# Kernel optimization log

Measured on AMD Instinct MI355X. Metric: run time of the kernel, lower is better.

Reference implementation:

```python
import jax, jax.numpy as jnp
import numpy as np

LOG2 = float(np.log(2.0))
CUTOFF = 10.0
INPUT_DIM = 5


def ssp(x):
    # ShiftedSoftplus
    return jax.nn.softplus(x) - LOG2


def setup_inputs() -> dict:
    key = jax.random.key(0)
    ks = jax.random.split(key, 16)
    N, E, D, G, L = 20000, 320000, 128, 100, 6
    s = 0.05
    return {
        "z": jax.random.normal(ks[0], (N, INPUT_DIM + D), jnp.float32),
        "edge_index": jax.random.randint(ks[1], (2, E), 0, N, dtype=jnp.int64),
        "edge_length": jax.random.uniform(ks[2], (E,), jnp.float32),
        "edge_attr": jax.random.uniform(ks[3], (E, G), jnp.float32),
        "emblin_w": jax.random.normal(ks[4], (D, INPUT_DIM), jnp.float32) * s,
        "emblin_b": jnp.zeros((D,), jnp.float32),
        "mlp_w1": jax.random.normal(ks[5], (L, D, G), jnp.float32) * s,
        "mlp_b1": jnp.zeros((L, D), jnp.float32),
        "mlp_w2": jax.random.normal(ks[6], (L, D, D), jnp.float32) * s,
        "mlp_b2": jnp.zeros((L, D), jnp.float32),
        "lin1_w": jax.random.normal(ks[7], (L, D, D), jnp.float32) * s,
        "lin2_w": jax.random.normal(ks[8], (L, D, D), jnp.float32) * s,
        "lin2_b": jnp.zeros((L, D), jnp.float32),
        "lin_w": jax.random.normal(ks[9], (L, D, 2 * D), jnp.float32) * s,
        "lin_b": jnp.zeros((L, D), jnp.float32),
    }


def reference(z, edge_index, edge_length, edge_attr, emblin_w, emblin_b,
              mlp_w1, mlp_b1, mlp_w2, mlp_b2, lin1_w, lin2_w, lin2_b,
              lin_w, lin_b):
    # time_emb=True path: split z into node features and time embedding
    zf, ptemb = z[:, :INPUT_DIM], z[:, INPUT_DIM:]
    h = zf @ emblin_w.T + emblin_b + ptemb          # [N, D]
    src, dst = edge_index[0], edge_index[1]
    N = h.shape[0]
    # non-smooth cutoff gate: C = (edge_length <= cutoff)
    C = (edge_length <= CUTOFF).astype(h.dtype)     # [E]
    L = mlp_w1.shape[0]
    for l in range(L):
        # edge-wise filter MLP with cutoff gate
        Wf = ssp(edge_attr @ mlp_w1[l].T + mlp_b1[l]) @ mlp_w2[l].T + mlp_b2[l]
        Wf = Wf * C[:, None]                        # [E, F]
        xf = h @ lin1_w[l].T                        # [N, F]
        m_ij = xf[src] * Wf                         # gather + elementwise, [E, F]
        m_i = jax.ops.segment_sum(m_ij, dst, num_segments=N)  # scatter-add, [N, F]
        m = ssp(m_i @ lin2_w[l].T + lin2_b[l])      # [N, D]
        h = h + (jnp.concatenate([h, m], axis=1) @ lin_w[l].T + lin_b[l])
    return h
```

## Files before the change

kernel.cpp:

```cpp
#include <hip/hip_runtime.h>

#define N_NODES 20000
#define D 128
#define E_EDGES 320000
#define G 100
#define L_LAYERS 6
#define IN_DIM 5
#define ZROW (IN_DIM + D)
#define CUTOFF_V 10.0f
#define LOG2F_ 0.69314718055994530942f

typedef __attribute__((ext_vector_type(8))) short bf16x8;
typedef __attribute__((ext_vector_type(4))) float f32x4;
typedef unsigned short ushort_t;
typedef unsigned int uint_t;

__device__ __forceinline__ float sspf(float x) {
    return fmaxf(x, 0.0f) + __logf(1.0f + __expf(-fabsf(x))) - LOG2F_;
}

__device__ __forceinline__ ushort_t f2bf(float f) {
    union { float f; uint_t u; } x; x.f = f;
    uint_t r = ((x.u >> 16) & 1u) + 0x7fffu;
    return (ushort_t)((x.u + r) >> 16);
}

__device__ __forceinline__ uint_t pack2(float a, float b) {
    return (uint_t)f2bf(a) | ((uint_t)f2bf(b) << 16);
}

__device__ __forceinline__ f32x4 mfma_bf16(bf16x8 a, bf16x8 b, f32x4 c) {
    return __builtin_amdgcn_mfma_f32_16x16x32_bf16(a, b, c, 0, 0, 0);
}

__global__ void embed_kernel(const float* __restrict__ z,
                             const float* __restrict__ ew,
                             const float* __restrict__ eb,
                             float* __restrict__ h) {
    int n = blockIdx.x;
    int d = threadIdx.x;
    const float* zr = z + (size_t)n * ZROW;
    float acc = eb[d] + zr[IN_DIM + d];
#pragma unroll
    for (int k = 0; k < IN_DIM; ++k) acc += zr[k] * ew[d * IN_DIM + k];
    h[(size_t)n * D + d] = acc;
}

__global__ void convw1_kernel(const float* __restrict__ w1, ushort_t* __restrict__ out) {
    int idx = blockIdx.x * 256 + threadIdx.x;
    int k = idx & 127;
    int nl = idx >> 7;
    out[idx] = (k < G) ? f2bf(w1[(size_t)nl * G + k]) : (ushort_t)0;
}

__global__ void castbf_kernel(const float* __restrict__ src, ushort_t* __restrict__ dst) {
    int i = blockIdx.x * 256 + threadIdx.x;
    dst[i] = f2bf(src[i]);
}

__global__ void hist_kernel(const int* __restrict__ ei, int* __restrict__ deg) {
    int e = blockIdx.x * 256 + threadIdx.x;
    atomicAdd(&deg[ei[E_EDGES + e]], 1);
}

__global__ __launch_bounds__(1024) void scan_kernel(const int* __restrict__ deg,
                                                    int* __restrict__ row_start,
                                                    int* __restrict__ cursor) {
    __shared__ int wsum[16];
    int t = threadIdx.x;
    const int CH = (N_NODES + 1023) / 1024;
    int base = t * CH;
    int s = 0;
    for (int i = 0; i < CH; ++i) {
        int idx = base + i;
        if (idx < N_NODES) s += deg[idx];
    }
    int lane = t & 63, wid = t >> 6;
    int v = s;
    for (int o = 1; o < 64; o <<= 1) {
        int u = __shfl_up(v, o, 64);
        if (lane >= o) v += u;
    }
    if (lane == 63) wsum[wid] = v;
    __syncthreads();
    if (t == 0) {
        int acc = 0;
        for (int i = 0; i < 16; ++i) { int tmp = wsum[i]; wsum[i] = acc; acc += tmp; }
    }
    __syncthreads();
    int run = v - s + wsum[wid];
    for (int i = 0; i < CH; ++i) {
        int idx = base + i;
        if (idx < N_NODES) {
            row_start[idx] = run;
            cursor[idx] = run;
            run += deg[idx];
        }
    }
    if (t == 0) row_start[N_NODES] = E_EDGES;
}

__global__ void scatter_perm_kernel(const int* __restrict__ ei, const float* __restrict__ el,
                                    int* __restrict__ cursor,
                                    int* __restrict__ perm, int* __restrict__ src_p,
                                    float* __restrict__ cm_p) {
    int e = blockIdx.x * 256 + threadIdx.x;
    int d = ei[E_EDGES + e];
    int p = atomicAdd(&cursor[d], 1);
    perm[p] = e;
    src_p[p] = ei[e];
    cm_p[p] = (el[e] <= CUTOFF_V) ? 1.0f : 0.0f;
}

__global__ void attr_perm_kernel(const float* __restrict__ edge_attr,
                                 const int* __restrict__ perm,
                                 ushort_t* __restrict__ attr_p) {
    int tid = blockIdx.x * 256 + threadIdx.x;
    int r = tid >> 5, ch = tid & 31;
    float4 v = make_float4(0.f, 0.f, 0.f, 0.f);
    if (ch < 25) {
        int pe = perm[r];
        v = *(const float4*)(edge_attr + (size_t)pe * G + ch * 4);
    }
    uint2 p; p.x = pack2(v.x, v.y); p.y = pack2(v.z, v.w);
    *(uint2*)(attr_p + (size_t)r * 128 + ch * 4) = p;
}

__global__ __launch_bounds__(256) void edge_mlp_kernel(
    const ushort_t* __restrict__ attr_p, const float* __restrict__ cm_p,
    const ushort_t* __restrict__ w1b, const float* __restrict__ b1,
    const ushort_t* __restrict__ w2b, const float* __restrict__ b2,
    ushort_t* __restrict__ wf) {
    __shared__ __align__(16) ushort_t sT[32][136];

    int t = threadIdx.x, lane = t & 63, wid = t >> 6;
    int c = lane & 15, quad = lane >> 4;
    int er0 = blockIdx.x * 32;
    int mbase = wid * 32;

    f32x4 acc[2][2];
#pragma unroll
    for (int st = 0; st < 2; ++st)
#pragma unroll
        for (int ct = 0; ct < 2; ++ct) acc[st][ct] = (f32x4){0.f, 0.f, 0.f, 0.f};

#pragma unroll
    for (int ks = 0; ks < 4; ++ks) {
        int koff = ks * 32 + quad * 8;
        bf16x8 b0  = *(const bf16x8*)(attr_p + (size_t)(er0 + c) * 128 + koff);
        bf16x8 b1v = *(const bf16x8*)(attr_p + (size_t)(er0 + 16 + c) * 128 + koff);
#pragma unroll
        for (int ct = 0; ct < 2; ++ct) {
            bf16x8 a = *(const bf16x8*)(w1b + (size_t)(mbase + ct * 16 + c) * 128 + koff);
            acc[0][ct] = mfma_bf16(a, b0, acc[0][ct]);
            acc[1][ct] = mfma_bf16(a, b1v, acc[1][ct]);
        }
    }
#pragma unroll
    for (int st = 0; st < 2; ++st)
#pragma unroll
        for (int ct = 0; ct < 2; ++ct) {
            int col = mbase + ct * 16 + quad * 4;
            float4 bv = *(const float4*)(b1 + col);
            uint2 p;
            p.x = pack2(sspf(acc[st][ct][0] + bv.x), sspf(acc[st][ct][1] + bv.y));
            p.y = pack2(sspf(acc[st][ct][2] + bv.z), sspf(acc[st][ct][3] + bv.w));
            *(uint2*)(&sT[st * 16 + c][col]) = p;
        }

    __syncthreads();

#pragma unroll
    for (int st = 0; st < 2; ++st)
#pragma unroll
        for (int ct = 0; ct < 2; ++ct) acc[st][ct] = (f32x4){0.f, 0.f, 0.f, 0.f};
#pragma unroll
    for (int ks = 0; ks < 4; ++ks) {
        int koff = ks * 32 + quad * 8;
        bf16x8 b0  = *(const bf16x8*)(&sT[c][koff]);
        bf16x8 b1v = *(const bf16x8*)(&sT[16 + c][koff]);
#pragma unroll
        for (int ct = 0; ct < 2; ++ct) {
            bf16x8 a = *(const bf16x8*)(w2b + (size_t)(mbase + ct * 16 + c) * 128 + koff);
            acc[0][ct] = mfma_bf16(a, b0, acc[0][ct]);
            acc[1][ct] = mfma_bf16(a, b1v, acc[1][ct]);
        }
    }
#pragma unroll
    for (int st = 0; st < 2; ++st) {
        int e = er0 + st * 16 + c;
        float cv = cm_p[e];
#pragma unroll
        for (int ct = 0; ct < 2; ++ct) {
            int col = mbase + ct * 16 + quad * 4;
            float4 bv = *(const float4*)(b2 + col);
            uint2 p;
            p.x = pack2((acc[st][ct][0] + bv.x) * cv, (acc[st][ct][1] + bv.y) * cv);
            p.y = pack2((acc[st][ct][2] + bv.z) * cv, (acc[st][ct][3] + bv.w) * cv);
            *(uint2*)(wf + (size_t)e * 128 + col) = p;
        }
    }
}

template <bool HASB, bool SSP, bool RES, bool BF16OUT, bool TWOK>
__global__ __launch_bounds__(256) void node_mfma_kernel(
    const float* __restrict__ in0, const float* __restrict__ in1,
    const ushort_t* __restrict__ Wb, const float* __restrict__ bias,
    const float* __restrict__ resid, void* __restrict__ outp) {
    __shared__ __align__(16) ushort_t sT[32][136];
    const int WS = TWOK ? 256 : 128;
    int t = threadIdx.x, lane = t & 63, wid = t >> 6;
    int c = lane & 15, quad = lane >> 4;
    int n0 = blockIdx.x * 32;
    int mbase = wid * 32;

    f32x4 acc[2][2];
#pragma unroll
    for (int st = 0; st < 2; ++st)
#pragma unroll
        for (int ct = 0; ct < 2; ++ct) acc[st][ct] = (f32x4){0.f, 0.f, 0.f, 0.f};

    const float* src = in0;
#pragma unroll 1
    for (int ph = 0; ph < (TWOK ? 2 : 1); ++ph) {
        if (ph) __syncthreads();
#pragma unroll
        for (int i = 0; i < 4; ++i) {
            int idx = i * 256 + t;
            int r = idx >> 5, ch = idx & 31;
            int gr = n0 + r;
            float4 v = make_float4(0.f, 0.f, 0.f, 0.f);
            if (gr < N_NODES) v = *(const float4*)(src + (size_t)gr * 128 + ch * 4);
            uint2 p; p.x = pack2(v.x, v.y); p.y = pack2(v.z, v.w);
            *(uint2*)(&sT[r][ch * 4]) = p;
        }
        __syncthreads();
        int kb = ph * 128;
#pragma unroll
        for (int ks = 0; ks < 4; ++ks) {
            int koff = ks * 32 + quad * 8;
            bf16x8 b0  = *(const bf16x8*)(&sT[c][koff]);
            bf16x8 b1v = *(const bf16x8*)(&sT[16 + c][koff]);
#pragma unroll
            for (int ct = 0; ct < 2; ++ct) {
                bf16x8 a = *(const bf16x8*)(Wb + (size_t)(mbase + ct * 16 + c) * WS + kb + koff);
                acc[0][ct] = mfma_bf16(a, b0, acc[0][ct]);
                acc[1][ct] = mfma_bf16(a, b1v, acc[1][ct]);
            }
        }
        src = in1;
    }

#pragma unroll
    for (int st = 0; st < 2; ++st) {
        int node = n0 + st * 16 + c;
        if (node < N_NODES) {
#pragma unroll
            for (int ct = 0; ct < 2; ++ct) {
                int col = mbase + ct * 16 + quad * 4;
                float4 bv = make_float4(0.f, 0.f, 0.f, 0.f);
                if (HASB) bv = *(const float4*)(bias + col);
                float v0 = acc[st][ct][0] + bv.x;
                float v1 = acc[st][ct][1] + bv.y;
                float v2 = acc[st][ct][2] + bv.z;
                float v3 = acc[st][ct][3] + bv.w;
                if (SSP) { v0 = sspf(v0); v1 = sspf(v1); v2 = sspf(v2); v3 = sspf(v3); }
                if (RES) {
                    float4 rv = *(const float4*)(resid + (size_t)node * 128 + col);
                    v0 += rv.x; v1 += rv.y; v2 += rv.z; v3 += rv.w;
                }
                if (BF16OUT) {
                    uint2 p; p.x = pack2(v0, v1); p.y = pack2(v2, v3);
                    *(uint2*)((ushort_t*)outp + (size_t)node * 128 + col) = p;
                } else {
                    *(float4*)((float*)outp + (size_t)node * 128 + col) =
                        make_float4(v0, v1, v2, v3);
                }
            }
        }
    }
}

__global__ __launch_bounds__(256) void segsum_kernel(
    const ushort_t* __restrict__ wf, const ushort_t* __restrict__ xf_bf,
    const int* __restrict__ row_start, const int* __restrict__ src_p,
    float* __restrict__ m_i) {
    int t = threadIdx.x, lane = t & 63;
    int n = blockIdx.x * 4 + (t >> 6);
    int beg = row_start[n], end = row_start[n + 1];
    float a0 = 0.f, a1 = 0.f;
    for (int i = beg; i < end; ++i) {
        uint_t w = *(const uint_t*)(wf + (size_t)i * 128 + lane * 2);
        uint_t x = *(const uint_t*)(xf_bf + (size_t)src_p[i] * 128 + lane * 2);
        a0 += __uint_as_float(w << 16) * __uint_as_float(x << 16);
        a1 += __uint_as_float(w & 0xffff0000u) * __uint_as_float(x & 0xffff0000u);
    }
    *(float2*)(m_i + (size_t)n * 128 + lane * 2) = make_float2(a0, a1);
}

extern "C" void kernel_launch(void* const* d_in, const int* in_sizes, int n_in,
                              void* d_out, int out_size, void* d_ws, size_t ws_size,
                              hipStream_t stream) {
    const float* z        = (const float*)d_in[0];
    const int*   ei       = (const int*)d_in[1];
    const float* el       = (const float*)d_in[2];
    const float* ea       = (const float*)d_in[3];
    const float* emblin_w = (const float*)d_in[4];
    const float* emblin_b = (const float*)d_in[5];
    const float* mlp_w1   = (const float*)d_in[6];
    const float* mlp_b1   = (const float*)d_in[7];
    const float* mlp_w2   = (const float*)d_in[8];
    const float* mlp_b2   = (const float*)d_in[9];
    const float* lin1_w   = (const float*)d_in[10];
    const float* lin2_w   = (const float*)d_in[11];
    const float* lin2_b   = (const float*)d_in[12];
    const float* lin_w    = (const float*)d_in[13];
    const float* lin_b    = (const float*)d_in[14];
    (void)in_sizes; (void)n_in; (void)out_size; (void)ws_size;

    const size_t ND = (size_t)N_NODES * D;
    float* ws   = (float*)d_ws;
    float* h    = ws;
    float* m_i  = h + ND;
    float* cm_p = m_i + ND;
    float* fend = cm_p + E_EDGES;

    ushort_t* w1b    = (ushort_t*)fend;
    ushort_t* w2b    = w1b   + (size_t)L_LAYERS * D * 128;
    ushort_t* lin1b  = w2b   + (size_t)L_LAYERS * D * D;
    ushort_t* lin2b  = lin1b + (size_t)L_LAYERS * D * D;
    ushort_t* linwb  = lin2b + (size_t)L_LAYERS * D * D;
    ushort_t* wf     = linwb + (size_t)L_LAYERS * D * 256;
    ushort_t* xf_bf  = wf    + (size_t)E_EDGES * 128;
    ushort_t* attr_p = xf_bf + ND;
    int* ibase      = (int*)(attr_p + (size_t)E_EDGES * 128);
    int* deg        = ibase;
    int* row_start  = deg + N_NODES;
    int* cursor     = row_start + N_NODES + 1;
    int* perm       = cursor + N_NODES;
    int* src_p      = perm + E_EDGES;

    convw1_kernel<<<(L_LAYERS * D * 128) / 256, 256, 0, stream>>>(mlp_w1, w1b);
    castbf_kernel<<<(L_LAYERS * D * D) / 256, 256, 0, stream>>>(mlp_w2, w2b);
    castbf_kernel<<<(L_LAYERS * D * D) / 256, 256, 0, stream>>>(lin1_w, lin1b);
    castbf_kernel<<<(L_LAYERS * D * D) / 256, 256, 0, stream>>>(lin2_w, lin2b);
    castbf_kernel<<<(L_LAYERS * D * 256) / 256, 256, 0, stream>>>(lin_w, linwb);

    hipMemsetAsync(deg, 0, (size_t)N_NODES * sizeof(int), stream);
    hist_kernel<<<E_EDGES / 256, 256, 0, stream>>>(ei, deg);
    scan_kernel<<<1, 1024, 0, stream>>>(deg, row_start, cursor);
    scatter_perm_kernel<<<E_EDGES / 256, 256, 0, stream>>>(ei, el, cursor, perm, src_p, cm_p);
    attr_perm_kernel<<<(E_EDGES * 32) / 256, 256, 0, stream>>>(ea, perm, attr_p);

    embed_kernel<<<N_NODES, D, 0, stream>>>(z, emblin_w, emblin_b, h);

    const int NBLK = (N_NODES + 31) / 32;
    for (int l = 0; l < L_LAYERS; ++l) {
        node_mfma_kernel<false, false, false, true, false><<<NBLK, 256, 0, stream>>>(
            h, nullptr, lin1b + (size_t)l * D * D, nullptr, nullptr, xf_bf);
        edge_mlp_kernel<<<E_EDGES / 32, 256, 0, stream>>>(
            attr_p, cm_p, w1b + (size_t)l * D * 128, mlp_b1 + (size_t)l * D,
            w2b + (size_t)l * D * D, mlp_b2 + (size_t)l * D, wf);
        segsum_kernel<<<N_NODES / 4, 256, 0, stream>>>(wf, xf_bf, row_start, src_p, m_i);
        node_mfma_kernel<true, true, false, false, false><<<NBLK, 256, 0, stream>>>(
            m_i, nullptr, lin2b + (size_t)l * D * D, lin2_b + (size_t)l * D,
            nullptr, m_i);
        node_mfma_kernel<true, false, true, false, true><<<NBLK, 256, 0, stream>>>(
            h, m_i, linwb + (size_t)l * D * 256, lin_b + (size_t)l * D, h, h);
    }

    hipMemcpyAsync(d_out, h, ND * sizeof(float), hipMemcpyDeviceToDevice, stream);
}
```

Baseline: 1.522 ms.

## Fuse lin2 and update GEMMs into one tail kernel; widen edge MLP waves

Merges the lin2+ssp node GEMM and the concat update GEMM into one kernel that keeps the ssp output in shared memory as bf16. This removes a kernel launch and the fp32 round trip of m_i through global memory. Separately, the edge MLP kernel now runs 2 waves of 128 threads, each covering 64 output columns instead of 32, so each block uses fewer threads and each thread holds more accumulators. In-place write of h is safe because each block reads only its own rows before writing them.

Result: faster. 1.401 ms (-8.0%).

```diff
diff --git a/kernel.cpp b/kernel.cpp
--- a/kernel.cpp
+++ b/kernel.cpp
@@ -126,7 +126,7 @@
     *(uint2*)(attr_p + (size_t)r * 128 + ch * 4) = p;
 }
 
-__global__ __launch_bounds__(256) void edge_mlp_kernel(
+__global__ __launch_bounds__(128) void edge_mlp_kernel(
     const ushort_t* __restrict__ attr_p, const float* __restrict__ cm_p,
     const ushort_t* __restrict__ w1b, const float* __restrict__ b1,
     const ushort_t* __restrict__ w2b, const float* __restrict__ b2,
@@ -136,13 +136,13 @@
     int t = threadIdx.x, lane = t & 63, wid = t >> 6;
     int c = lane & 15, quad = lane >> 4;
     int er0 = blockIdx.x * 32;
-    int mbase = wid * 32;
-
-    f32x4 acc[2][2];
-#pragma unroll
-    for (int st = 0; st < 2; ++st)
-#pragma unroll
-        for (int ct = 0; ct < 2; ++ct) acc[st][ct] = (f32x4){0.f, 0.f, 0.f, 0.f};
+    int mbase = wid * 64;
+
+    f32x4 acc[2][4];
+#pragma unroll
+    for (int st = 0; st < 2; ++st)
+#pragma unroll
+        for (int ct = 0; ct < 4; ++ct) acc[st][ct] = (f32x4){0.f, 0.f, 0.f, 0.f};
 
 #pragma unroll
     for (int ks = 0; ks < 4; ++ks) {
@@ -150,7 +150,7 @@
         bf16x8 b0  = *(const bf16x8*)(attr_p + (size_t)(er0 + c) * 128 + koff);
         bf16x8 b1v = *(const bf16x8*)(attr_p + (size_t)(er0 + 16 + c) * 128 + koff);
 #pragma unroll
-        for (int ct = 0; ct < 2; ++ct) {
+        for (int ct = 0; ct < 4; ++ct) {
             bf16x8 a = *(const bf16x8*)(w1b + (size_t)(mbase + ct * 16 + c) * 128 + koff);
             acc[0][ct] = mfma_bf16(a, b0, acc[0][ct]);
             acc[1][ct] = mfma_bf16(a, b1v, acc[1][ct]);
@@ -159,7 +159,7 @@
 #pragma unroll
     for (int st = 0; st < 2; ++st)
 #pragma unroll
-        for (int ct = 0; ct < 2; ++ct) {
+        for (int ct = 0; ct < 4; ++ct) {
             int col = mbase + ct * 16 + quad * 4;
             float4 bv = *(const float4*)(b1 + col);
             uint2 p;
@@ -173,14 +173,14 @@
 #pragma unroll
     for (int st = 0; st < 2; ++st)
 #pragma unroll
-        for (int ct = 0; ct < 2; ++ct) acc[st][ct] = (f32x4){0.f, 0.f, 0.f, 0.f};
+        for (int ct = 0; ct < 4; ++ct) acc[st][ct] = (f32x4){0.f, 0.f, 0.f, 0.f};
 #pragma unroll
     for (int ks = 0; ks < 4; ++ks) {
         int koff = ks * 32 + quad * 8;
         bf16x8 b0  = *(const bf16x8*)(&sT[c][koff]);
         bf16x8 b1v = *(const bf16x8*)(&sT[16 + c][koff]);
 #pragma unroll
-        for (int ct = 0; ct < 2; ++ct) {
+        for (int ct = 0; ct < 4; ++ct) {
             bf16x8 a = *(const bf16x8*)(w2b + (size_t)(mbase + ct * 16 + c) * 128 + koff);
             acc[0][ct] = mfma_bf16(a, b0, acc[0][ct]);
             acc[1][ct] = mfma_bf16(a, b1v, acc[1][ct]);
@@ -191,7 +191,7 @@
         int e = er0 + st * 16 + c;
         float cv = cm_p[e];
 #pragma unroll
-        for (int ct = 0; ct < 2; ++ct) {
+        for (int ct = 0; ct < 4; ++ct) {
             int col = mbase + ct * 16 + quad * 4;
             float4 bv = *(const float4*)(b2 + col);
             uint2 p;
@@ -202,13 +202,10 @@
     }
 }
 
-template <bool HASB, bool SSP, bool RES, bool BF16OUT, bool TWOK>
-__global__ __launch_bounds__(256) void node_mfma_kernel(
-    const float* __restrict__ in0, const float* __restrict__ in1,
-    const ushort_t* __restrict__ Wb, const float* __restrict__ bias,
-    const float* __restrict__ resid, void* __restrict__ outp) {
+__global__ __launch_bounds__(256) void lin1_kernel(
+    const float* __restrict__ in0, const ushort_t* __restrict__ Wb,
+    ushort_t* __restrict__ outp) {
     __shared__ __align__(16) ushort_t sT[32][136];
-    const int WS = TWOK ? 256 : 128;
     int t = threadIdx.x, lane = t & 63, wid = t >> 6;
     int c = lane & 15, quad = lane >> 4;
     int n0 = blockIdx.x * 32;
@@ -220,35 +217,28 @@
 #pragma unroll
         for (int ct = 0; ct < 2; ++ct) acc[st][ct] = (f32x4){0.f, 0.f, 0.f, 0.f};
 
-    const float* src = in0;
-#pragma unroll 1
-    for (int ph = 0; ph < (TWOK ? 2 : 1); ++ph) {
-        if (ph) __syncthreads();
-#pragma unroll
-        for (int i = 0; i < 4; ++i) {
-            int idx = i * 256 + t;
-            int r = idx >> 5, ch = idx & 31;
-            int gr = n0 + r;
-            float4 v = make_float4(0.f, 0.f, 0.f, 0.f);
-            if (gr < N_NODES) v = *(const float4*)(src + (size_t)gr * 128 + ch * 4);
-            uint2 p; p.x = pack2(v.x, v.y); p.y = pack2(v.z, v.w);
-            *(uint2*)(&sT[r][ch * 4]) = p;
-        }
-        __syncthreads();
-        int kb = ph * 128;
-#pragma unroll
-        for (int ks = 0; ks < 4; ++ks) {
-            int koff = ks * 32 + quad * 8;
-            bf16x8 b0  = *(const bf16x8*)(&sT[c][koff]);
-            bf16x8 b1v = *(const bf16x8*)(&sT[16 + c][koff]);
-#pragma unroll
-            for (int ct = 0; ct < 2; ++ct) {
-                bf16x8 a = *(const bf16x8*)(Wb + (size_t)(mbase + ct * 16 + c) * WS + kb + koff);
-                acc[0][ct] = mfma_bf16(a, b0, acc[0][ct]);
-                acc[1][ct] = mfma_bf16(a, b1v, acc[1][ct]);
-            }
-        }
-        src = in1;
+#pragma unroll
+    for (int i = 0; i < 4; ++i) {
+        int idx = i * 256 + t;
+        int r = idx >> 5, ch = idx & 31;
+        int gr = n0 + r;
+        float4 v = make_float4(0.f, 0.f, 0.f, 0.f);
+        if (gr < N_NODES) v = *(const float4*)(in0 + (size_t)gr * 128 + ch * 4);
+        uint2 p; p.x = pack2(v.x, v.y); p.y = pack2(v.z, v.w);
+        *(uint2*)(&sT[r][ch * 4]) = p;
+    }
+    __syncthreads();
+#pragma unroll
+    for (int ks = 0; ks < 4; ++ks) {
+        int koff = ks * 32 + quad * 8;
+        bf16x8 b0  = *(const bf16x8*)(&sT[c][koff]);
+        bf16x8 b1v = *(const bf16x8*)(&sT[16 + c][koff]);
+#pragma unroll
+        for (int ct = 0; ct < 2; ++ct) {
+            bf16x8 a = *(const bf16x8*)(Wb + (size_t)(mbase + ct * 16 + c) * 128 + koff);
+            acc[0][ct] = mfma_bf16(a, b0, acc[0][ct]);
+            acc[1][ct] = mfma_bf16(a, b1v, acc[1][ct]);
+        }
     }
 
 #pragma unroll
@@ -258,24 +248,123 @@
 #pragma unroll
             for (int ct = 0; ct < 2; ++ct) {
                 int col = mbase + ct * 16 + quad * 4;
-                float4 bv = make_float4(0.f, 0.f, 0.f, 0.f);
-                if (HASB) bv = *(const float4*)(bias + col);
-                float v0 = acc[st][ct][0] + bv.x;
-                float v1 = acc[st][ct][1] + bv.y;
-                float v2 = acc[st][ct][2] + bv.z;
-                float v3 = acc[st][ct][3] + bv.w;
-                if (SSP) { v0 = sspf(v0); v1 = sspf(v1); v2 = sspf(v2); v3 = sspf(v3); }
-                if (RES) {
-                    float4 rv = *(const float4*)(resid + (size_t)node * 128 + col);
-                    v0 += rv.x; v1 += rv.y; v2 += rv.z; v3 += rv.w;
-                }
-                if (BF16OUT) {
-                    uint2 p; p.x = pack2(v0, v1); p.y = pack2(v2, v3);
-                    *(uint2*)((ushort_t*)outp + (size_t)node * 128 + col) = p;
-                } else {
-                    *(float4*)((float*)outp + (size_t)node * 128 + col) =
-                        make_float4(v0, v1, v2, v3);
-                }
+                uint2 p;
+                p.x = pack2(acc[st][ct][0], acc[st][ct][1]);
+                p.y = pack2(acc[st][ct][2], acc[st][ct][3]);
+                *(uint2*)(outp + (size_t)node * 128 + col) = p;
+            }
+        }
+    }
+}
+
+__global__ __launch_bounds__(256) void fused_tail_kernel(
+    const float* __restrict__ m_in, const float* __restrict__ h,
+    const ushort_t* __restrict__ W2b, const float* __restrict__ b2,
+    const ushort_t* __restrict__ Wub, const float* __restrict__ bu,
+    float* __restrict__ h_out) {
+    __shared__ __align__(16) ushort_t sT[32][136];
+    __shared__ __align__(16) ushort_t sM[32][136];
+    int t = threadIdx.x, lane = t & 63, wid = t >> 6;
+    int c = lane & 15, quad = lane >> 4;
+    int n0 = blockIdx.x * 32;
+    int mbase = wid * 32;
+
+    f32x4 acc[2][2];
+#pragma unroll
+    for (int st = 0; st < 2; ++st)
+#pragma unroll
+        for (int ct = 0; ct < 2; ++ct) acc[st][ct] = (f32x4){0.f, 0.f, 0.f, 0.f};
+
+#pragma unroll
+    for (int i = 0; i < 4; ++i) {
+        int idx = i * 256 + t;
+        int r = idx >> 5, ch = idx & 31;
+        int gr = n0 + r;
+        float4 v = make_float4(0.f, 0.f, 0.f, 0.f);
+        if (gr < N_NODES) v = *(const float4*)(m_in + (size_t)gr * 128 + ch * 4);
+        uint2 p; p.x = pack2(v.x, v.y); p.y = pack2(v.z, v.w);
+        *(uint2*)(&sT[r][ch * 4]) = p;
+    }
+    __syncthreads();
+#pragma unroll
+    for (int ks = 0; ks < 4; ++ks) {
+        int koff = ks * 32 + quad * 8;
+        bf16x8 b0  = *(const bf16x8*)(&sT[c][koff]);
+        bf16x8 b1v = *(const bf16x8*)(&sT[16 + c][koff]);
+#pragma unroll
+        for (int ct = 0; ct < 2; ++ct) {
+            bf16x8 a = *(const bf16x8*)(W2b + (size_t)(mbase + ct * 16 + c) * 128 + koff);
+            acc[0][ct] = mfma_bf16(a, b0, acc[0][ct]);
+            acc[1][ct] = mfma_bf16(a, b1v, acc[1][ct]);
+        }
+    }
+#pragma unroll
+    for (int st = 0; st < 2; ++st)
+#pragma unroll
+        for (int ct = 0; ct < 2; ++ct) {
+            int col = mbase + ct * 16 + quad * 4;
+            float4 bv = *(const float4*)(b2 + col);
+            uint2 p;
+            p.x = pack2(sspf(acc[st][ct][0] + bv.x), sspf(acc[st][ct][1] + bv.y));
+            p.y = pack2(sspf(acc[st][ct][2] + bv.z), sspf(acc[st][ct][3] + bv.w));
+            *(uint2*)(&sM[st * 16 + c][col]) = p;
+        }
+    __syncthreads();
+
+#pragma unroll
+    for (int i = 0; i < 4; ++i) {
+        int idx = i * 256 + t;
+        int r = idx >> 5, ch = idx & 31;
+        int gr = n0 + r;
+        float4 v = make_float4(0.f, 0.f, 0.f, 0.f);
+        if (gr < N_NODES) v = *(const float4*)(h + (size_t)gr * 128 + ch * 4);
+        uint2 p; p.x = pack2(v.x, v.y); p.y = pack2(v.z, v.w);
+        *(uint2*)(&sT[r][ch * 4]) = p;
+    }
+    __syncthreads();
+#pragma unroll
+    for (int st = 0; st < 2; ++st)
+#pragma unroll
+        for (int ct = 0; ct < 2; ++ct) acc[st][ct] = (f32x4){0.f, 0.f, 0.f, 0.f};
+#pragma unroll
+    for (int ks = 0; ks < 4; ++ks) {
+        int koff = ks * 32 + quad * 8;
+        bf16x8 b0  = *(const bf16x8*)(&sT[c][koff]);
+        bf16x8 b1v = *(const bf16x8*)(&sT[16 + c][koff]);
+#pragma unroll
+        for (int ct = 0; ct < 2; ++ct) {
+            bf16x8 a = *(const bf16x8*)(Wub + (size_t)(mbase + ct * 16 + c) * 256 + koff);
+            acc[0][ct] = mfma_bf16(a, b0, acc[0][ct]);
+            acc[1][ct] = mfma_bf16(a, b1v, acc[1][ct]);
+        }
+    }
+#pragma unroll
+    for (int ks = 0; ks < 4; ++ks) {
+        int koff = ks * 32 + quad * 8;
+        bf16x8 b0  = *(const bf16x8*)(&sM[c][koff]);
+        bf16x8 b1v = *(const bf16x8*)(&sM[16 + c][koff]);
+#pragma unroll
+        for (int ct = 0; ct < 2; ++ct) {
+            bf16x8 a = *(const bf16x8*)(Wub + (size_t)(mbase + ct * 16 + c) * 256 + 128 + koff);
+            acc[0][ct] = mfma_bf16(a, b0, acc[0][ct]);
+            acc[1][ct] = mfma_bf16(a, b1v, acc[1][ct]);
+        }
+    }
+#pragma unroll
+    for (int st = 0; st < 2; ++st) {
+        int node = n0 + st * 16 + c;
+        if (node < N_NODES) {
+#pragma unroll
+            for (int ct = 0; ct < 2; ++ct) {
+                int col = mbase + ct * 16 + quad * 4;
+                float4 bv = *(const float4*)(bu + col);
+                float4 rv = *(const float4*)(h + (size_t)node * 128 + col);
+                float4 o;
+                o.x = acc[st][ct][0] + bv.x + rv.x;
+                o.y = acc[st][ct][1] + bv.y + rv.y;
+                o.z = acc[st][ct][2] + bv.z + rv.z;
+                o.w = acc[st][ct][3] + bv.w + rv.w;
+                *(float4*)(h_out + (size_t)node * 128 + col) = o;
             }
         }
     }
@@ -356,17 +445,14 @@
 
     const int NBLK = (N_NODES + 31) / 32;
     for (int l = 0; l < L_LAYERS; ++l) {
-        node_mfma_kernel<false, false, false, true, false><<<NBLK, 256, 0, stream>>>(
-            h, nullptr, lin1b + (size_t)l * D * D, nullptr, nullptr, xf_bf);
-        edge_mlp_kernel<<<E_EDGES / 32, 256, 0, stream>>>(
+        lin1_kernel<<<NBLK, 256, 0, stream>>>(h, lin1b + (size_t)l * D * D, xf_bf);
+        edge_mlp_kernel<<<E_EDGES / 32, 128, 0, stream>>>(
             attr_p, cm_p, w1b + (size_t)l * D * 128, mlp_b1 + (size_t)l * D,
             w2b + (size_t)l * D * D, mlp_b2 + (size_t)l * D, wf);
         segsum_kernel<<<N_NODES / 4, 256, 0, stream>>>(wf, xf_bf, row_start, src_p, m_i);
-        node_mfma_kernel<true, true, false, false, false><<<NBLK, 256, 0, stream>>>(
-            m_i, nullptr, lin2b + (size_t)l * D * D, lin2_b + (size_t)l * D,
-            nullptr, m_i);
-        node_mfma_kernel<true, false, true, false, true><<<NBLK, 256, 0, stream>>>(
-            h, m_i, linwb + (size_t)l * D * 256, lin_b + (size_t)l * D, h, h);
+        fused_tail_kernel<<<NBLK, 256, 0, stream>>>(
+            m_i, h, lin2b + (size_t)l * D * D, lin2_b + (size_t)l * D,
+            linwb + (size_t)l * D * 256, lin_b + (size_t)l * D, h);
     }
 
     hipMemcpyAsync(d_out, h, ND * sizeof(float), hipMemcpyDeviceToDevice, stream);
```
